# Optimization experiments

Measured on AMD Instinct MI355X. Metric: run time of the kernel, lower is better.

Reference implementation:

```python
import jax, jax.numpy as jnp
import numpy as np

N_WIRES = 10
N_OPS = 30
C64 = jnp.complex64

# Frozen random circuit (stand-in for tq.RandomLayer(n_ops=30)): deterministic op list.
_rng = np.random.default_rng(42)
OPS = []
for _ in range(N_OPS):
    k = int(_rng.integers(0, 4))
    if k == 3:
        w = _rng.choice(N_WIRES, size=2, replace=False)
        OPS.append(('cnot', int(w[0]), int(w[1])))
    else:
        OPS.append((('rx', 'ry', 'rz')[k], int(_rng.integers(0, N_WIRES)), -1))


def _rx_mat(t):
    c = jnp.cos(t / 2).astype(C64)
    s = jnp.sin(t / 2).astype(C64)
    return jnp.stack([jnp.stack([c, -1j * s]), jnp.stack([-1j * s, c])])


def _ry_mat(t):
    c = jnp.cos(t / 2).astype(C64)
    s = jnp.sin(t / 2).astype(C64)
    return jnp.stack([jnp.stack([c, -s]), jnp.stack([s, c])])


def _rz_mat(t):
    tc = t.astype(C64)
    z = jnp.zeros((), C64)
    return jnp.stack([jnp.stack([jnp.exp(-1j * tc / 2), z]), jnp.stack([z, jnp.exp(1j * tc / 2)])])

_GATE = {'rx': _rx_mat, 'ry': _ry_mat, 'rz': _rz_mat}


def _apply_1q(state, U, w):
    # state: [bsz] + [2]*N_WIRES ; apply 2x2 U on qubit axis w
    s = jnp.moveaxis(state, 1 + w, -1)
    s = jnp.einsum('ij,...j->...i', U, s)
    return jnp.moveaxis(s, -1, 1 + w)


def _apply_cnot(state, c, t):
    s = jnp.moveaxis(state, (1 + c, 1 + t), (-2, -1))
    s = jnp.stack([s[..., 0, :], s[..., 1, ::-1]], axis=-2)  # flip target when control=1
    return jnp.moveaxis(s, (-2, -1), (1 + c, 1 + t))


def _quantum_head(x, rand_params, rx_theta, ry_theta, head_w, head_b):
    bsz = x.shape[0]
    # GeneralEncoder '10xRy': RY(x[:,w])|0> per wire -> product state built directly
    state = jnp.ones((bsz, 1), C64)
    for w in range(N_WIRES):
        vec = jnp.stack([jnp.cos(x[:, w] / 2), jnp.sin(x[:, w] / 2)], axis=-1).astype(C64)
        state = (state[:, :, None] * vec[:, None, :]).reshape(bsz, -1)
    state = state.reshape((bsz,) + (2,) * N_WIRES)
    # RandomLayer (frozen 30-op circuit, one angle per op)
    for i, (kind, a, b) in enumerate(OPS):
        if kind == 'cnot':
            state = _apply_cnot(state, a, b)
        else:
            state = _apply_1q(state, _GATE[kind](rand_params[i]), a)
    # shared trainable RX then RY applied to every wire (single shared param each)
    Urx = _rx_mat(rx_theta[0])
    Ury = _ry_mat(ry_theta[0])
    for w in range(N_WIRES):
        state = _apply_1q(state, Urx, w)
        state = _apply_1q(state, Ury, w)
    # MeasureAll(PauliZ): <Z_w> = P(bit_w=0) - P(bit_w=1)
    probs = jnp.abs(state) ** 2  # float32, [bsz] + [2]*n
    feats = []
    for w in range(N_WIRES):
        axes = tuple(1 + q for q in range(N_WIRES) if q != w)
        p = probs.sum(axis=axes)  # [bsz, 2]
        feats.append(p[:, 0] - p[:, 1])
    feats = jnp.stack(feats, axis=-1)  # [bsz, n_wires]
    return feats @ head_w + head_b[0]


def _mlp(x, w0, b0, w1, b1, w2, b2, w3, b3):
    # faithful to ClassicalMLP: Linear chain with NO activations
    h = x @ w0.T + b0
    h = h @ w1.T + b1
    h = h @ w2.T + b2
    return (h @ w3.T + b3)[:, 0]


def setup_inputs() -> dict:
    key = jax.random.key(0)
    ks = jax.random.split(key, 14)
    BSZ = 8192
    return {
        'state_batch': jax.random.normal(ks[0], (BSZ, N_WIRES), jnp.float32),
        'rand_params': jax.random.normal(ks[1], (N_OPS,), jnp.float32),
        'rx_theta': jax.random.normal(ks[2], (1,), jnp.float32),
        'ry_theta': jax.random.normal(ks[3], (1,), jnp.float32),
        'head_w': jax.random.normal(ks[4], (N_WIRES,), jnp.float32) * 0.3,
        'head_b': jax.random.normal(ks[5], (1,), jnp.float32) * 0.1,
        'w0': jax.random.normal(ks[6], (64, N_WIRES), jnp.float32) * 0.3,
        'b0': jax.random.normal(ks[7], (64,), jnp.float32) * 0.1,
        'w1': jax.random.normal(ks[8], (32, 64), jnp.float32) * 0.12,
        'b1': jax.random.normal(ks[9], (32,), jnp.float32) * 0.1,
        'w2': jax.random.normal(ks[10], (16, 32), jnp.float32) * 0.17,
        'b2': jax.random.normal(ks[11], (16,), jnp.float32) * 0.1,
        'w3': jax.random.normal(ks[12], (1, 16), jnp.float32) * 0.25,
        'b3': jax.random.normal(ks[13], (1,), jnp.float32) * 0.1,
    }


def reference(state_batch, rand_params, rx_theta, ry_theta, head_w, head_b, w0, b0, w1, b1, w2, b2, w3, b3):
    q = _quantum_head(state_batch, rand_params, rx_theta, ry_theta, head_w, head_b)
    c = _mlp(state_batch, w0, b0, w1, b1, w2, b2, w3, b3)
    return q + c
```

## Files before the change

kernel.cpp:

```cpp
#include <hip/hip_runtime.h>
#include <cstdint>

#define NW 10
#define NOPS 30

namespace {

typedef unsigned __int128 u128;

struct CRng { u128 state; u128 inc; bool has32; uint32_t cached; };

constexpr u128 PCG_MUL = (((u128)0x2360ED051FC65DA4ULL) << 64) | (u128)0x4385DF649FCCF645ULL;

constexpr void cr_step(CRng &r) { r.state = r.state * PCG_MUL + r.inc; }

constexpr uint64_t cr_out(u128 st) {
  uint64_t hi = (uint64_t)(st >> 64);
  uint64_t lo = (uint64_t)st;
  unsigned rot = (unsigned)(st >> 122) & 63u;
  uint64_t v = hi ^ lo;
  return (v >> rot) | (v << ((64u - rot) & 63u));
}

constexpr uint64_t cr_next64(CRng &r) { cr_step(r); return cr_out(r.state); }

constexpr uint32_t cr_next32(CRng &r) {
  if (r.has32) { r.has32 = false; return r.cached; }
  uint64_t v = cr_next64(r);
  r.has32 = true; r.cached = (uint32_t)(v >> 32);
  return (uint32_t)v;
}

constexpr CRng cr_seed(uint32_t ent) {
  uint32_t pool[4] = {0u, 0u, 0u, 0u};
  uint32_t hc = 0x43b0d7e5u;
  for (int i = 0; i < 4; i++) {
    uint32_t v = (i == 0) ? ent : 0u;
    v ^= hc; hc *= 0x931e8875u; v *= hc; v ^= v >> 16;
    pool[i] = v;
  }
  for (int s = 0; s < 4; s++)
    for (int d = 0; d < 4; d++)
      if (s != d) {
        uint32_t v = pool[s];
        v ^= hc; hc *= 0x931e8875u; v *= hc; v ^= v >> 16;
        uint32_t res = 0xca01f9ddu * pool[d] - 0x4973f715u * v;
        res ^= res >> 16;
        pool[d] = res;
      }
  uint32_t hb = 0x8b51f9ddu;
  uint64_t s64[4] = {0ull, 0ull, 0ull, 0ull};
  for (int i = 0; i < 8; i++) {
    uint32_t d = pool[i & 3];
    d ^= hb; hb *= 0x58f38dedu; d *= hb; d ^= d >> 16;
    if (i & 1) s64[i >> 1] |= ((uint64_t)d << 32); else s64[i >> 1] = (uint64_t)d;
  }
  CRng r{};
  u128 initstate = (((u128)s64[0]) << 64) | (u128)s64[1];
  u128 initseq   = (((u128)s64[2]) << 64) | (u128)s64[3];
  r.state = 0; r.inc = (initseq << 1) | (u128)1;
  cr_step(r);
  r.state += initstate;
  cr_step(r);
  r.has32 = false; r.cached = 0u;
  return r;
}

constexpr uint32_t cr_lemire32(CRng &r, uint32_t rng) {
  uint32_t rng_excl = rng + 1u;
  uint64_t m = (uint64_t)cr_next32(r) * (uint64_t)rng_excl;
  uint32_t leftover = (uint32_t)m;
  if (leftover < rng_excl) {
    uint32_t threshold = (uint32_t)(0xFFFFFFFFu - rng) % rng_excl;
    while (leftover < threshold) {
      m = (uint64_t)cr_next32(r) * (uint64_t)rng_excl;
      leftover = (uint32_t)m;
    }
  }
  return (uint32_t)(m >> 32);
}

constexpr bool canary_pcg42() {
  CRng r = cr_seed(42u);
  double a = (double)(cr_next64(r) >> 11) * (1.0 / 9007199254740992.0);
  double b = (double)(cr_next64(r) >> 11) * (1.0 / 9007199254740992.0);
  double c = (double)(cr_next64(r) >> 11) * (1.0 / 9007199254740992.0);
  bool ok = (a > 0.77395603) && (a < 0.77395607);
  ok = ok && (b > 0.43887842) && (b < 0.43887846);
  ok = ok && (c > 0.85859790) && (c < 0.85859794);
  return ok;
}
static_assert(canary_pcg42(), "CANARY_PCG_SEED42_RANDOM_MISMATCH");

struct COp { int kind; int a; int b; int slot; };
struct Circ { COp op[NOPS]; };

constexpr Circ build_circuit() {
  Circ c{};
  CRng r = cr_seed(42u);
  for (int i = 0; i < NOPS; i++) {
    int k = (int)cr_lemire32(r, 3u);
    if (k == 3) {
      uint32_t v8 = cr_lemire32(r, 8u);
      uint32_t v9 = cr_lemire32(r, 9u);
      uint32_t i0 = v8;
      uint32_t i1 = (v9 == v8) ? 9u : v9;
      uint32_t j = cr_lemire32(r, 1u);
      if (j == 0u) { uint32_t t = i0; i0 = i1; i1 = t; }
      c.op[i] = COp{3, (int)i0, (int)i1, i};
    } else {
      int w = (int)cr_lemire32(r, 9u);
      c.op[i] = COp{k, w, 0, i};
    }
  }
  return c;
}
constexpr Circ CC = build_circuit();

constexpr int MAXP = 16384;
constexpr int MAXU = 4096;

struct Tables {
  int np, nu, overflow;
  uint32_t pmeta[MAXP]; uint32_t pcm[MAXP]; uint32_t psm[MAXP];
  uint32_t ukey[MAXU];  int ustart[MAXU + 1];
  uint32_t upk[MAXU];
  uint32_t pa[MAXP]; uint32_t pb[MAXP]; uint16_t pu[MAXP];
};

constexpr Tables build_tables() {
  Tables T{};
  uint32_t meta[MAXP] = {}; uint32_t cm[MAXP] = {}; uint32_t sm[MAXP] = {};
  int np = 0; int ovf = 0;
  for (int w = 0; w < NW; w++)
    for (int src = 0; src < 3; src++) {
      uint32_t xm = (src != 0) ? (1u << w) : 0u;
      uint32_t zm = (src != 1) ? (1u << w) : 0u;
      meta[np] = xm | (zm << 10) | ((uint32_t)w << 21) | ((uint32_t)src << 25);
      cm[np] = 0u; sm[np] = 0u; np++;
    }
  for (int k = NOPS - 1; k >= 0 && !ovf; k--) {
    const COp op = CC.op[k];
    if (op.kind == 3) {
      const int c = op.a, t = op.b;
      for (int p = 0; p < np; p++) {
        uint32_t m = meta[p];
        uint32_t xm = m & 1023u, zm = (m >> 10) & 1023u;
        uint32_t xc = (xm >> c) & 1u, zc = (zm >> c) & 1u;
        uint32_t xt = (xm >> t) & 1u, zt = (zm >> t) & 1u;
        uint32_t fl = xc & zt & (1u ^ (xt ^ zc));
        xm ^= xc << t;
        zm ^= zt << c;
        m = (m & ~(1023u | (1023u << 10))) | xm | (zm << 10);
        m ^= fl << 20;
        meta[p] = m;
      }
    } else {
      const int q = op.a, ax = op.kind, bit = op.slot;
      const int n0 = np;
      for (int p = 0; p < n0; p++) {
        uint32_t m = meta[p];
        uint32_t x = (m >> q) & 1u;
        uint32_t z = (m >> (10 + q)) & 1u;
        uint32_t viol = (ax == 0) ? z : (ax == 1) ? (x ^ z) : x;
        if (viol) {
          uint32_t nx = 0, nz = 0, fl = 0;
          if (ax == 0)      { if (x) { nx = 0; nz = 1; fl = 1; } else { nx = 1; nz = 1; fl = 0; } }
          else if (ax == 1) { if (x) { nx = 0; nz = 1; fl = 0; } else { nx = 1; nz = 0; fl = 1; } }
          else              { if (z) { nx = 1; nz = 0; fl = 0; } else { nx = 1; nz = 1; fl = 1; } }
          if (np >= MAXP) { ovf = 1; break; }
          uint32_t m2 = m;
          m2 &= ~((1u << q) | (1u << (10 + q)));
          m2 |= (nx << q) | (nz << (10 + q));
          m2 ^= fl << 20;
          meta[np] = m2; cm[np] = cm[p]; sm[np] = sm[p] | (1u << bit);
          np++;
          cm[p] |= 1u << bit;
        }
      }
    }
  }
  if (ovf) { T.overflow = 1; return T; }
  int n2 = 0;
  for (int p = 0; p < np; p++) {
    uint32_t m = meta[p];
    if ((m & 1023u) & ((m >> 10) & 1023u)) continue;
    meta[n2] = m; cm[n2] = cm[p]; sm[n2] = sm[p]; n2++;
  }
  np = n2;
  int idx[MAXP] = {}; int tmp[MAXP] = {};
  for (int i = 0; i < np; i++) idx[i] = i;
  int hist[1025] = {};
  for (int i = 0; i < 1025; i++) hist[i] = 0;
  for (int i = 0; i < np; i++) hist[1 + (meta[idx[i]] & 1023u)]++;
  for (int i = 0; i < 1024; i++) hist[i + 1] += hist[i];
  for (int i = 0; i < np; i++) tmp[hist[meta[idx[i]] & 1023u]++] = idx[i];
  for (int i = 0; i < 1025; i++) hist[i] = 0;
  for (int i = 0; i < np; i++) hist[1 + ((meta[tmp[i]] >> 10) & 1023u)]++;
  for (int i = 0; i < 1024; i++) hist[i + 1] += hist[i];
  for (int i = 0; i < np; i++) idx[hist[(meta[tmp[i]] >> 10) & 1023u]++] = tmp[i];
  uint16_t puTmp[MAXP] = {};
  int nu = 0; uint32_t prev = 0xFFFFFFFFu;
  for (int i = 0; i < np; i++) {
    int p = idx[i];
    uint32_t key = meta[p] & 0xFFFFFu;
    if (key != prev) {
      if (nu >= MAXU) { T.overflow = 2; return T; }
      T.ukey[nu] = key; T.ustart[nu] = i; prev = key; nu++;
    }
    T.pmeta[i] = meta[p]; T.pcm[i] = cm[p]; T.psm[i] = sm[p];
    puTmp[i] = (uint16_t)(nu - 1);
  }
  T.ustart[nu] = np;
  for (int u = 0; u < nu; u++) {
    uint32_t key = T.ukey[u]; uint32_t pk = 0;
    for (int p = 0; p < 5; p++) {
      uint32_t x2 = (key >> (2 * p)) & 3u;
      uint32_t z2 = (key >> (10 + 2 * p)) & 3u;
      pk |= ((x2 | (z2 << 2)) << 2) << (6 * p);
    }
    T.upk[u] = pk;
  }
  int P = 997;
  {
    bool ok = false;
    while (!ok) {
      int a = P, b = np;
      while (b) { int t2 = a % b; a = b; b = t2; }
      if (a == 1) ok = true; else P++;
    }
  }
  constexpr int POW3[5] = {1, 3, 9, 27, 81};
  for (int j = 0; j < np; j++) {
    int i = (int)(((long long)j * P) % np);
    uint32_t cmv = T.pcm[i], smv = T.psm[i], m = T.pmeta[i];
    uint32_t g[6] = {0, 0, 0, 0, 0, 0};
    uint32_t mm = cmv;
    while (mm) { int b = __builtin_ctz(mm); mm &= mm - 1u; g[b / 5] += (uint32_t)POW3[b % 5]; }
    mm = smv;
    while (mm) { int b = __builtin_ctz(mm); mm &= mm - 1u; g[b / 5] += 2u * (uint32_t)POW3[b % 5]; }
    T.pa[j] = g[0] | (g[1] << 8) | (g[2] << 16) | (g[3] << 24);
    T.pb[j] = g[4] | (g[5] << 8) | (((m >> 21) & 15u) << 16)
            | (((m >> 25) & 3u) << 20) | (((m >> 20) & 1u) << 22);
    T.pu[j] = puTmp[i];
  }
  T.np = np; T.nu = nu; T.overflow = 0;
  return T;
}

constexpr Tables TT = build_tables();
static_assert(TT.overflow == 0, "PAULI_PATH_OVERFLOW_raise_MAXP_or_pivot_to_runtime_tables");
static_assert(TT.nu >= 1 && TT.nu <= MAXU, "PAULI_UNIQUE_COUNT_OUT_OF_RANGE");
constexpr int NU  = TT.nu;
constexpr int NUP = (NU + 1) & ~1;
constexpr int NP  = TT.np;

}

__device__ const Tables dTT = TT;

#define BLOCK 1024
#define WPB   16
#define PWRK  (BLOCK - 16)

__global__ __launch_bounds__(BLOCK) void fused_kernel(
    const float* __restrict__ x,
    const float* __restrict__ rand_params,
    const float* __restrict__ rx_theta, const float* __restrict__ ry_theta,
    const float* __restrict__ head_w, const float* __restrict__ head_b,
    const float* __restrict__ w0, const float* __restrict__ b0,
    const float* __restrict__ w1, const float* __restrict__ b1,
    const float* __restrict__ w2, const float* __restrict__ b2,
    const float* __restrict__ w3, const float* __restrict__ b3,
    float* __restrict__ out, int bsz)
{
  __shared__ __align__(16) float2 CKsh[NUP];
  __shared__ float Gt[6 * 243];
  __shared__ float Tbl[WPB][80];
  __shared__ float ct[32], st[32], abr[3], hwsh[10];
  __shared__ float r2[32], r1[64];
  __shared__ float MLPsh[NW + 1];

  const int tid  = threadIdx.x;
  const int wave = tid >> 6;
  const int lane = tid & 63;

  const int wv = blockIdx.x * WPB + wave;
  const bool live = (wv < bsz);
  const float* xe = x + wv * NW;
  float* tbl = Tbl[wave];

  if (tid < NOPS) {
    float t = rand_params[tid];
    ct[tid] = cosf(t);
    st[tid] = sinf(t);
  } else if (tid == 32) {
    float tx = rx_theta[0], ty = ry_theta[0];
    abr[0] = cosf(tx) * cosf(ty);
    abr[1] = -sinf(ty);
    abr[2] = sinf(tx) * cosf(ty);
  } else if (tid >= 40 && tid < 40 + NW) {
    hwsh[tid - 40] = head_w[tid - 40];
  } else if (tid >= 64 && tid < 96) {
    const int j = tid - 64;
    float acc = 0.f;
    for (int k = 0; k < 16; k++) acc += w3[k] * w2[k * 32 + j];
    r2[j] = acc;
  }
  for (int i = tid; i < NUP; i += BLOCK)
    CKsh[i] = make_float2(0.f, __uint_as_float(i < NU ? dTT.upk[i] : 0u));
  if (live) {
    {
      const int e = lane;
      const int p = e >> 4, code = e & 15;
      float2 xv = *(const float2*)(xe + 2 * p);
      float c0 = __cosf(xv.x), s0 = __sinf(xv.x);
      float c1 = __cosf(xv.y), s1 = __sinf(xv.y);
      float f0 = (code & 1) ? s0 : ((code & 4) ? c0 : 1.0f);
      float f1 = (code & 2) ? s1 : ((code & 8) ? c1 : 1.0f);
      tbl[e] = f0 * f1;
    }
    if (lane < 16) {
      const int e = lane + 64;
      const int p = e >> 4, code = e & 15;
      float2 xv = *(const float2*)(xe + 2 * p);
      float c0 = __cosf(xv.x), s0 = __sinf(xv.x);
      float c1 = __cosf(xv.y), s1 = __sinf(xv.y);
      float f0 = (code & 1) ? s0 : ((code & 4) ? c0 : 1.0f);
      float f1 = (code & 2) ? s1 : ((code & 8) ? c1 : 1.0f);
      tbl[e] = f0 * f1;
    }
  }
  __syncthreads();

  for (int e = tid; e < 6 * 243; e += BLOCK) {
    const int g = e / 243;
    int c = e - g * 243;
    float v = 1.f;
#pragma unroll
    for (int j = 0; j < 5; j++) {
      int tr = c % 3; c /= 3;
      if (tr == 1) v *= ct[5 * g + j];
      else if (tr == 2) v *= st[5 * g + j];
    }
    Gt[e] = v;
  }
  if (tid >= BLOCK - 64) {
    const int j = tid - (BLOCK - 64);
    float acc = 0.f;
    for (int k = 0; k < 32; k++) acc += r2[k] * w1[k * 64 + j];
    r1[j] = acc;
  }
  __syncthreads();

  if (tid < NW) {
    float acc = 0.f;
    for (int k = 0; k < 64; k++) acc += r1[k] * w0[k * NW + tid];
    MLPsh[tid] = acc;
  } else if (tid == NW) {
    float acc = b3[0] + head_b[0];
    for (int k = 0; k < 16; k++) acc += w3[k] * b2[k];
    for (int k = 0; k < 32; k++) acc += r2[k] * b1[k];
    for (int k = 0; k < 64; k++) acc += r1[k] * b0[k];
    MLPsh[NW] = acc;
  } else if (tid >= 16) {
    for (int i = tid - 16; i < NP; i += PWRK) {
      uint32_t pa = dTT.pa[i];
      uint32_t pb = dTT.pb[i];
      int      u  = (int)dTT.pu[i];
      float v = hwsh[(pb >> 16) & 15u] * abr[(pb >> 20) & 3u];
      if (pb & (1u << 22)) v = -v;
      v *= Gt[         (pa       ) & 255u] * Gt[1 * 243 + ((pa >>  8) & 255u)];
      v *= Gt[2 * 243 + ((pa >> 16) & 255u)] * Gt[3 * 243 + ( pa >> 24        )];
      v *= Gt[4 * 243 + ( pb        & 255u)] * Gt[5 * 243 + ((pb >>  8) & 255u)];
      atomicAdd(&CKsh[u].x, v);
    }
  }
  __syncthreads();
  if (!live) return;

  const char* tb = (const char*)tbl;
  float acc0 = 0.f, acc1 = 0.f;
#pragma unroll 4
  for (int s = 2 * lane; s < NUP; s += 128) {
    float4 q = *(const float4*)&CKsh[s];
    uint32_t ka = __float_as_uint(q.y);
    uint32_t kb = __float_as_uint(q.w);
    float a0 = *(const float*)(tb +       ( ka        & 63u));
    float a1 = *(const float*)(tb +  64 + ((ka >>  6) & 63u));
    float a2 = *(const float*)(tb + 128 + ((ka >> 12) & 63u));
    float a3 = *(const float*)(tb + 192 + ((ka >> 18) & 63u));
    float a4 = *(const float*)(tb + 256 + ((ka >> 24) & 63u));
    float b0v = *(const float*)(tb +       ( kb        & 63u));
    float b1v = *(const float*)(tb +  64 + ((kb >>  6) & 63u));
    float b2v = *(const float*)(tb + 128 + ((kb >> 12) & 63u));
    float b3v = *(const float*)(tb + 192 + ((kb >> 18) & 63u));
    float b4v = *(const float*)(tb + 256 + ((kb >> 24) & 63u));
    acc0 = fmaf(q.x, ((a0 * a1) * (a2 * a3)) * a4, acc0);
    acc1 = fmaf(q.z, ((b0v * b1v) * (b2v * b3v)) * b4v, acc1);
  }
  float acc = acc0 + acc1;

#pragma unroll
  for (int m = 1; m < 64; m <<= 1) acc += __shfl_xor(acc, m);

  if (lane == 0) {
    float cc = MLPsh[NW];
#pragma unroll
    for (int w = 0; w < NW; w++) cc += xe[w] * MLPsh[w];
    out[wv] = acc + cc;
  }
}

extern "C" void kernel_launch(void* const* d_in, const int* in_sizes, int n_in,
                              void* d_out, int out_size, void* d_ws, size_t ws_size,
                              hipStream_t stream) {
  const float* x   = (const float*)d_in[0];
  const float* rp  = (const float*)d_in[1];
  const float* rxT = (const float*)d_in[2];
  const float* ryT = (const float*)d_in[3];
  const float* hw  = (const float*)d_in[4];
  const float* hb  = (const float*)d_in[5];
  const float* w0  = (const float*)d_in[6];
  const float* b0  = (const float*)d_in[7];
  const float* w1  = (const float*)d_in[8];
  const float* b1  = (const float*)d_in[9];
  const float* w2  = (const float*)d_in[10];
  const float* b2  = (const float*)d_in[11];
  const float* w3  = (const float*)d_in[12];
  const float* b3  = (const float*)d_in[13];
  const int bsz = in_sizes[0] / NW;

  const int blocks = (bsz + WPB - 1) / WPB;
  hipLaunchKernelGGL(fused_kernel, dim3(blocks), dim3(BLOCK), 0, stream,
                     x, rp, rxT, ryT, hw, hb, w0, b0, w1, b1, w2, b2, w3, b3,
                     (float*)d_out, bsz);
}
```

Measured before the change: 91.51 us.

## Process two batch rows per wave to amortize per-block coefficient setup

Each wave now evaluates two batch elements, so a 1024-thread block covers 32 rows instead of 16 and the grid is halved. The per-block cost of building the Pauli-coefficient table (the atomics pass over all paths) and the MLP folding is therefore amortized over twice as many rows, and each CKsh entry loaded from LDS feeds two rows. The pa/pb path tables are also interleaved into a single array so each path is fetched with one 8-byte load. The trade-off is more registers and LDS gathers per wave, plus longer serial work per block with fewer blocks to spread across CUs.

Result: faster. 86.24 us (-5.8%).

```diff
diff --git a/kernel.cpp b/kernel.cpp
--- a/kernel.cpp
+++ b/kernel.cpp
@@ -125,7 +125,7 @@
   uint32_t pmeta[MAXP]; uint32_t pcm[MAXP]; uint32_t psm[MAXP];
   uint32_t ukey[MAXU];  int ustart[MAXU + 1];
   uint32_t upk[MAXU];
-  uint32_t pa[MAXP]; uint32_t pb[MAXP]; uint16_t pu[MAXP];
+  uint32_t pab[2 * MAXP]; uint16_t pu[MAXP];
 };
 
 constexpr Tables build_tables() {
@@ -239,9 +239,9 @@
     while (mm) { int b = __builtin_ctz(mm); mm &= mm - 1u; g[b / 5] += (uint32_t)POW3[b % 5]; }
     mm = smv;
     while (mm) { int b = __builtin_ctz(mm); mm &= mm - 1u; g[b / 5] += 2u * (uint32_t)POW3[b % 5]; }
-    T.pa[j] = g[0] | (g[1] << 8) | (g[2] << 16) | (g[3] << 24);
-    T.pb[j] = g[4] | (g[5] << 8) | (((m >> 21) & 15u) << 16)
-            | (((m >> 25) & 3u) << 20) | (((m >> 20) & 1u) << 22);
+    T.pab[2 * j]     = g[0] | (g[1] << 8) | (g[2] << 16) | (g[3] << 24);
+    T.pab[2 * j + 1] = g[4] | (g[5] << 8) | (((m >> 21) & 15u) << 16)
+                     | (((m >> 25) & 3u) << 20) | (((m >> 20) & 1u) << 22);
     T.pu[j] = puTmp[i];
   }
   T.np = np; T.nu = nu; T.overflow = 0;
@@ -260,7 +260,7 @@
 __device__ const Tables dTT = TT;
 
 #define BLOCK 1024
-#define WPB   16
+#define WPB   32
 #define PWRK  (BLOCK - 16)
 
 __global__ __launch_bounds__(BLOCK) void fused_kernel(
@@ -285,10 +285,14 @@
   const int wave = tid >> 6;
   const int lane = tid & 63;
 
-  const int wv = blockIdx.x * WPB + wave;
-  const bool live = (wv < bsz);
-  const float* xe = x + wv * NW;
-  float* tbl = Tbl[wave];
+  const int wvA = blockIdx.x * WPB + 2 * wave;
+  const int wvB = wvA + 1;
+  const bool liveA = (wvA < bsz);
+  const bool liveB = (wvB < bsz);
+  const float* xeA = x + wvA * NW;
+  const float* xeB = x + wvB * NW;
+  float* tblA = Tbl[2 * wave];
+  float* tblB = Tbl[2 * wave + 1];
 
   if (tid < NOPS) {
     float t = rand_params[tid];
@@ -309,26 +313,48 @@
   }
   for (int i = tid; i < NUP; i += BLOCK)
     CKsh[i] = make_float2(0.f, __uint_as_float(i < NU ? dTT.upk[i] : 0u));
-  if (live) {
+  if (liveA) {
     {
       const int e = lane;
       const int p = e >> 4, code = e & 15;
-      float2 xv = *(const float2*)(xe + 2 * p);
+      float2 xv = *(const float2*)(xeA + 2 * p);
       float c0 = __cosf(xv.x), s0 = __sinf(xv.x);
       float c1 = __cosf(xv.y), s1 = __sinf(xv.y);
       float f0 = (code & 1) ? s0 : ((code & 4) ? c0 : 1.0f);
       float f1 = (code & 2) ? s1 : ((code & 8) ? c1 : 1.0f);
-      tbl[e] = f0 * f1;
+      tblA[e] = f0 * f1;
     }
     if (lane < 16) {
       const int e = lane + 64;
       const int p = e >> 4, code = e & 15;
-      float2 xv = *(const float2*)(xe + 2 * p);
+      float2 xv = *(const float2*)(xeA + 2 * p);
       float c0 = __cosf(xv.x), s0 = __sinf(xv.x);
       float c1 = __cosf(xv.y), s1 = __sinf(xv.y);
       float f0 = (code & 1) ? s0 : ((code & 4) ? c0 : 1.0f);
       float f1 = (code & 2) ? s1 : ((code & 8) ? c1 : 1.0f);
-      tbl[e] = f0 * f1;
+      tblA[e] = f0 * f1;
+    }
+  }
+  if (liveB) {
+    {
+      const int e = lane;
+      const int p = e >> 4, code = e & 15;
+      float2 xv = *(const float2*)(xeB + 2 * p);
+      float c0 = __cosf(xv.x), s0 = __sinf(xv.x);
+      float c1 = __cosf(xv.y), s1 = __sinf(xv.y);
+      float f0 = (code & 1) ? s0 : ((code & 4) ? c0 : 1.0f);
+      float f1 = (code & 2) ? s1 : ((code & 8) ? c1 : 1.0f);
+      tblB[e] = f0 * f1;
+    }
+    if (lane < 16) {
+      const int e = lane + 64;
+      const int p = e >> 4, code = e & 15;
+      float2 xv = *(const float2*)(xeB + 2 * p);
+      float c0 = __cosf(xv.x), s0 = __sinf(xv.x);
+      float c1 = __cosf(xv.y), s1 = __sinf(xv.y);
+      float f0 = (code & 1) ? s0 : ((code & 4) ? c0 : 1.0f);
+      float f1 = (code & 2) ? s1 : ((code & 8) ? c1 : 1.0f);
+      tblB[e] = f0 * f1;
     }
   }
   __syncthreads();
@@ -364,9 +390,10 @@
     for (int k = 0; k < 64; k++) acc += r1[k] * b0[k];
     MLPsh[NW] = acc;
   } else if (tid >= 16) {
+#pragma unroll 2
     for (int i = tid - 16; i < NP; i += PWRK) {
-      uint32_t pa = dTT.pa[i];
-      uint32_t pb = dTT.pb[i];
+      uint2 pp = *(const uint2*)&dTT.pab[2 * i];
+      uint32_t pa = pp.x, pb = pp.y;
       int      u  = (int)dTT.pu[i];
       float v = hwsh[(pb >> 16) & 15u] * abr[(pb >> 20) & 3u];
       if (pb & (1u << 22)) v = -v;
@@ -377,38 +404,57 @@
     }
   }
   __syncthreads();
-  if (!live) return;
-
-  const char* tb = (const char*)tbl;
-  float acc0 = 0.f, acc1 = 0.f;
+  if (!liveA) return;
+
+  const char* tA = (const char*)tblA;
+  const char* tB = (const char*)tblB;
+  float aA0 = 0.f, aA1 = 0.f, aB0 = 0.f, aB1 = 0.f;
 #pragma unroll 4
   for (int s = 2 * lane; s < NUP; s += 128) {
     float4 q = *(const float4*)&CKsh[s];
     uint32_t ka = __float_as_uint(q.y);
     uint32_t kb = __float_as_uint(q.w);
-    float a0 = *(const float*)(tb +       ( ka        & 63u));
-    float a1 = *(const float*)(tb +  64 + ((ka >>  6) & 63u));
-    float a2 = *(const float*)(tb + 128 + ((ka >> 12) & 63u));
-    float a3 = *(const float*)(tb + 192 + ((ka >> 18) & 63u));
-    float a4 = *(const float*)(tb + 256 + ((ka >> 24) & 63u));
-    float b0v = *(const float*)(tb +       ( kb        & 63u));
-    float b1v = *(const float*)(tb +  64 + ((kb >>  6) & 63u));
-    float b2v = *(const float*)(tb + 128 + ((kb >> 12) & 63u));
-    float b3v = *(const float*)(tb + 192 + ((kb >> 18) & 63u));
-    float b4v = *(const float*)(tb + 256 + ((kb >> 24) & 63u));
-    acc0 = fmaf(q.x, ((a0 * a1) * (a2 * a3)) * a4, acc0);
-    acc1 = fmaf(q.z, ((b0v * b1v) * (b2v * b3v)) * b4v, acc1);
-  }
-  float acc = acc0 + acc1;
+    uint32_t o0 =  ka        & 63u, o1 = (ka >>  6) & 63u, o2 = (ka >> 12) & 63u,
+             o3 = (ka >> 18) & 63u, o4 = (ka >> 24) & 63u;
+    uint32_t p0 =  kb        & 63u, p1 = (kb >>  6) & 63u, p2 = (kb >> 12) & 63u,
+             p3 = (kb >> 18) & 63u, p4 = (kb >> 24) & 63u;
+    float fA0 = *(const float*)(tA + o0) * *(const float*)(tA + 64 + o1)
+              * *(const float*)(tA + 128 + o2) * *(const float*)(tA + 192 + o3)
+              * *(const float*)(tA + 256 + o4);
+    float fA1 = *(const float*)(tA + p0) * *(const float*)(tA + 64 + p1)
+              * *(const float*)(tA + 128 + p2) * *(const float*)(tA + 192 + p3)
+              * *(const float*)(tA + 256 + p4);
+    float fB0 = *(const float*)(tB + o0) * *(const float*)(tB + 64 + o1)
+              * *(const float*)(tB + 128 + o2) * *(const float*)(tB + 192 + o3)
+              * *(const float*)(tB + 256 + o4);
+    float fB1 = *(const float*)(tB + p0) * *(const float*)(tB + 64 + p1)
+              * *(const float*)(tB + 128 + p2) * *(const float*)(tB + 192 + p3)
+              * *(const float*)(tB + 256 + p4);
+    aA0 = fmaf(q.x, fA0, aA0);
+    aA1 = fmaf(q.z, fA1, aA1);
+    aB0 = fmaf(q.x, fB0, aB0);
+    aB1 = fmaf(q.z, fB1, aB1);
+  }
+  float accA = aA0 + aA1;
+  float accB = aB0 + aB1;
 
 #pragma unroll
-  for (int m = 1; m < 64; m <<= 1) acc += __shfl_xor(acc, m);
+  for (int m = 1; m < 64; m <<= 1) {
+    accA += __shfl_xor(accA, m);
+    accB += __shfl_xor(accB, m);
+  }
 
   if (lane == 0) {
-    float cc = MLPsh[NW];
+    float ccA = MLPsh[NW];
 #pragma unroll
-    for (int w = 0; w < NW; w++) cc += xe[w] * MLPsh[w];
-    out[wv] = acc + cc;
+    for (int w = 0; w < NW; w++) ccA += xeA[w] * MLPsh[w];
+    out[wvA] = accA + ccA;
+    if (liveB) {
+      float ccB = MLPsh[NW];
+#pragma unroll
+      for (int w = 0; w < NW; w++) ccB += xeB[w] * MLPsh[w];
+      out[wvB] = accB + ccB;
+    }
   }
 }
 
```
